# Performance work log

Measured on AMD Instinct MI355X. Metric: run time of the kernel, lower is better.

Reference implementation:

```python
import jax, jax.numpy as jnp
import numpy as np

B, T, E, H = 4, 1024, 1024, 16
D = E // H  # head_dim = 64


def setup_inputs() -> dict:
    key = jax.random.key(0)
    ks = jax.random.split(key, 6)
    s = 0.02  # realistic init scale for stable softmax
    return {
        "hidden_states": jax.random.normal(ks[0], (B, T, E), jnp.float32),
        "attention_mask": jnp.zeros((B, 1, T, T), jnp.float32),
        "Wq": jax.random.normal(ks[1], (E, E), jnp.float32) * s,
        "bq": jnp.zeros((E,), jnp.float32),
        "Wk": jax.random.normal(ks[2], (E, E), jnp.float32) * s,
        "bk": jnp.zeros((E,), jnp.float32),
        "Wv": jax.random.normal(ks[3], (E, E), jnp.float32) * s,
        "bv": jnp.zeros((E,), jnp.float32),
        "Wo": jax.random.normal(ks[4], (E, E), jnp.float32) * s,
        "bo": jnp.zeros((E,), jnp.float32),
    }


def reference(hidden_states, attention_mask, Wq, bq, Wk, bk, Wv, bv, Wo, bo):
    b, t, e = hidden_states.shape
    scaling = jnp.asarray(D, hidden_states.dtype) ** -0.5
    # q_proj weights/bias are pre-scaled in the module; equivalent to scaling q output
    q = (hidden_states @ Wq.T + bq) * scaling      # [B,T,E]
    k = hidden_states @ Wk.T + bk                   # self-attention path (no cache)
    v = hidden_states @ Wv.T + bv
    q = q.reshape(b, t, H, D)
    k = k.reshape(b, t, H, D)
    v = v.reshape(b, t, H, D)
    # bmm(q, k^T): [B,H,T,S] score matrix (materialized, as in the original)
    scores = jnp.einsum("bthd,bshd->bhts", q, k) + attention_mask
    probs = jax.nn.softmax(scores, axis=-1)
    ctx = jnp.einsum("bhts,bshd->bthd", probs, v).reshape(b, t, e)
    return ctx @ Wo.T + bo
```

## Files before the change

kernel.cpp:

```cpp
#include <hip/hip_runtime.h>
#include <math.h>

#define BB 4
#define TT 1024
#define EE 1024
#define HH 16
#define DD 64
#define KDIM 1024
#define N_HS (4096 * 1024)
#define N_W  (1024 * 1024)
#define NQKV (BB * HH * TT * DD)
#define LOG2E 1.44269504088896340736f

typedef _Float16 f16x8 __attribute__((ext_vector_type(8)));
typedef _Float16 f16x4 __attribute__((ext_vector_type(4)));
typedef _Float16 f16x2 __attribute__((ext_vector_type(2)));
typedef float    f32x4 __attribute__((ext_vector_type(4)));

__device__ __forceinline__ unsigned short f2h(float x) {
    _Float16 h = (_Float16)x;
    return __builtin_bit_cast(unsigned short, h);
}
__device__ __forceinline__ void split_h(float x, unsigned short& hi, unsigned short& lo) {
    _Float16 h = (_Float16)x;
    hi = __builtin_bit_cast(unsigned short, h);
    lo = f2h(x - (float)h);
}

__device__ __forceinline__ f16x2 cvt_pk(float a, float b) {
    return __builtin_bit_cast(f16x2, __builtin_amdgcn_cvt_pkrtz(a, b));
}

__device__ __forceinline__ void gload16(const void* g, void* l) {
    __builtin_amdgcn_global_load_lds(
        (const __attribute__((address_space(1))) void*)g,
        (__attribute__((address_space(3))) void*)l, 16, 0, 0);
}

__device__ __forceinline__ float mx3(float a, float b, float c) {
    return fmaxf(fmaxf(a, b), c);
}

__global__ __launch_bounds__(256)
void split_kernel(const float* __restrict__ hs,
                  const float* __restrict__ Wq, const float* __restrict__ Wk,
                  const float* __restrict__ Wv, const float* __restrict__ Wo,
                  const float* __restrict__ mask, int* __restrict__ mflag,
                  unsigned short* __restrict__ ws)
{
    const int u = blockIdx.x * 256 + threadIdx.x;
    if (u < (N_HS / 4) + N_W) {
        const float* src;
        unsigned short* dst;
        if (u < (N_HS / 4)) {
            src = hs + (size_t)u * 4;
            dst = ws + (size_t)u * 4;
        } else {
            int v = u - N_HS / 4;
            int wsel = v >> 18;
            int wo   = v & 0x3FFFF;
            const float* Wsrc = (wsel == 0) ? Wq : (wsel == 1) ? Wk : (wsel == 2) ? Wv : Wo;
            src = Wsrc + (size_t)wo * 4;
            dst = ws + (size_t)N_HS + (size_t)wsel * N_W + (size_t)wo * 4;
        }
        float4 x = *(const float4*)src;
        ushort4 h4;
        h4.x = f2h(x.x); h4.y = f2h(x.y); h4.z = f2h(x.z); h4.w = f2h(x.w);
        *(ushort4*)dst = h4;
    } else {
        int v = u - ((N_HS / 4) + N_W);
        float4 x = *(const float4*)(mask + (size_t)v * 4);
        bool nz = (x.x != 0.f) || (x.y != 0.f) || (x.z != 0.f) || (x.w != 0.f);
        if (__any(nz) && (threadIdx.x & 63) == 0)
            atomicOr(mflag, 1);
    }
}

__global__ __launch_bounds__(256)
void qkv_kernel(const unsigned short* __restrict__ hsp,
                const unsigned short* __restrict__ wqp,
                const float* __restrict__ bq, const float* __restrict__ bk,
                const float* __restrict__ bv,
                unsigned short* __restrict__ qkvb,
                unsigned short* __restrict__ vtp)
{
    __shared__ unsigned short Ah[128 * 32], Bh[128 * 32];
    __shared__ unsigned short Ts[128 * 128];

    const int widx  = blockIdx.x >> 3;
    const int nbase = (blockIdx.x & 7) * 128;
    const int mbase = blockIdx.y * 128;
    const unsigned short* Wp = wqp + (size_t)widx * N_W;
    const float* bias = (widx == 0) ? bq : (widx == 1) ? bk : bv;
    unsigned short* dst = qkvb + (size_t)widx * NQKV;
    const float scale = (widx == 0) ? 0.125f * LOG2E : 1.0f;

    const int tid  = threadIdx.x;
    const int w    = tid >> 6;
    const int lane = tid & 63;
    const int quad = lane >> 4;
    const int l16  = lane & 15;
    const int wm   = (w >> 1) * 64;
    const int wn   = (w & 1) * 64;

    f32x4 acc[4][4];
#pragma unroll
    for (int i = 0; i < 4; i++)
#pragma unroll
        for (int j = 0; j < 4; j++) acc[i][j] = (f32x4)0.f;

#pragma unroll 1
    for (int kt = 0; kt < KDIM; kt += 32) {
        __syncthreads();
#pragma unroll
        for (int i = 0; i < 2; i++) {
            int u = tid + i * 256;
            int r = u >> 2, c = u & 3;
            int q = c ^ ((r >> 1) & 3);
            gload16(hsp + (size_t)(mbase + r) * KDIM + kt + q * 8, &Ah[u * 8]);
            gload16(Wp  + (size_t)(nbase + r) * KDIM + kt + q * 8, &Bh[u * 8]);
        }
        __syncthreads();

        f16x8 af[4], bfr[4];
#pragma unroll
        for (int i = 0; i < 4; i++) {
            int r = wm + i * 16 + l16;
            af[i] = *(const f16x8*)&Ah[(r * 4 + (quad ^ ((r >> 1) & 3))) * 8];
        }
#pragma unroll
        for (int j = 0; j < 4; j++) {
            int r = wn + j * 16 + l16;
            bfr[j] = *(const f16x8*)&Bh[(r * 4 + (quad ^ ((r >> 1) & 3))) * 8];
        }
#pragma unroll
        for (int i = 0; i < 4; i++)
#pragma unroll
            for (int j = 0; j < 4; j++)
                acc[i][j] = __builtin_amdgcn_mfma_f32_16x16x32_f16(af[i], bfr[j], acc[i][j], 0, 0, 0);
    }

    if (widx == 2) {
#pragma unroll
        for (int j = 0; j < 4; j++) {
            int n = wn + j * 16 + l16;
            float bj = bias[nbase + n];
            int x = (n & 15) << 2;
#pragma unroll
            for (int i = 0; i < 4; i++) {
                int t4 = wm + i * 16 + quad * 4;
                ushort4 vw;
                vw.x = f2h(acc[i][j][0] + bj);
                vw.y = f2h(acc[i][j][1] + bj);
                vw.z = f2h(acc[i][j][2] + bj);
                vw.w = f2h(acc[i][j][3] + bj);
                *(ushort4*)&Ts[n * 128 + (t4 ^ x)] = vw;
            }
        }
        __syncthreads();
        const int b  = mbase >> 10;
        const int tb = mbase & 1023;
#pragma unroll
        for (int e = 0; e < 8; e++) {
            int c  = tid + e * 256;
            int n  = c >> 4, ch = c & 15;
            int x  = (n & 15) << 2;
            int s  = ch * 8;
            uint2 a0 = *(const uint2*)&Ts[n * 128 + (s ^ x)];
            uint2 a1 = *(const uint2*)&Ts[n * 128 + ((s + 4) ^ x)];
            int nn = nbase + n;
            int h = nn >> 6, d = nn & 63;
            uint4 o;
            o.x = a0.x; o.y = a0.y; o.z = a1.x; o.w = a1.y;
            *(uint4*)(vtp + (((size_t)(b * HH + h) * DD + d) * TT + tb + s)) = o;
        }
    } else {
#pragma unroll
        for (int j = 0; j < 4; j++) {
            int n = nbase + wn + j * 16 + l16;
            int h = n >> 6, d = n & 63;
            float bj = bias[n];
#pragma unroll
            for (int i = 0; i < 4; i++)
#pragma unroll
                for (int rr = 0; rr < 4; rr++) {
                    int m = mbase + wm + i * 16 + quad * 4 + rr;
                    int b = m >> 10, t = m & 1023;
                    dst[(((size_t)(b * HH + h) * TT + t) * DD + d)] =
                        f2h((acc[i][j][rr] + bj) * scale);
                }
        }
    }
}

__global__ __launch_bounds__(256)
void outproj_kernel(const unsigned short* __restrict__ ctxh,
                    const unsigned short* __restrict__ ctxl,
                    const unsigned short* __restrict__ wop,
                    const float* __restrict__ bo, float* __restrict__ out)
{
    __shared__ unsigned short Ach[64 * 32], Acl[64 * 32], Bh[128 * 32];

    const int nbase = blockIdx.x * 128;
    const int mbase = blockIdx.y * 64;

    const int tid  = threadIdx.x;
    const int w    = tid >> 6;
    const int lane = tid & 63;
    const int quad = lane >> 4;
    const int l16  = lane & 15;
    const int wm   = (w >> 1) * 32;
    const int wn   = (w & 1) * 64;

    f32x4 acc[2][4];
#pragma unroll
    for (int i = 0; i < 2; i++)
#pragma unroll
        for (int j = 0; j < 4; j++) acc[i][j] = (f32x4)0.f;

#pragma unroll 1
    for (int kt = 0; kt < KDIM; kt += 32) {
        __syncthreads();
        {
            int r = tid >> 2, c = tid & 3;
            int q = c ^ ((r >> 1) & 3);
            size_t ga = (size_t)(mbase + r) * KDIM + kt + q * 8;
            gload16(ctxh + ga, &Ach[tid * 8]);
            gload16(ctxl + ga, &Acl[tid * 8]);
        }
#pragma unroll
        for (int i = 0; i < 2; i++) {
            int u = tid + i * 256;
            int r = u >> 2, c = u & 3;
            int q = c ^ ((r >> 1) & 3);
            gload16(wop + (size_t)(nbase + r) * KDIM + kt + q * 8, &Bh[u * 8]);
        }
        __syncthreads();

        f16x8 ah[2], al[2], bfr[4];
#pragma unroll
        for (int i = 0; i < 2; i++) {
            int r = wm + i * 16 + l16;
            int slot = (r * 4 + (quad ^ ((r >> 1) & 3))) * 8;
            ah[i] = *(const f16x8*)&Ach[slot];
            al[i] = *(const f16x8*)&Acl[slot];
        }
#pragma unroll
        for (int j = 0; j < 4; j++) {
            int r = wn + j * 16 + l16;
            bfr[j] = *(const f16x8*)&Bh[(r * 4 + (quad ^ ((r >> 1) & 3))) * 8];
        }
#pragma unroll
        for (int i = 0; i < 2; i++)
#pragma unroll
            for (int j = 0; j < 4; j++) {
                acc[i][j] = __builtin_amdgcn_mfma_f32_16x16x32_f16(ah[i], bfr[j], acc[i][j], 0, 0, 0);
                acc[i][j] = __builtin_amdgcn_mfma_f32_16x16x32_f16(al[i], bfr[j], acc[i][j], 0, 0, 0);
            }
    }

#pragma unroll
    for (int j = 0; j < 4; j++) {
        int n = nbase + wn + j * 16 + l16;
        float bj = bo[n];
#pragma unroll
        for (int i = 0; i < 2; i++)
#pragma unroll
            for (int rr = 0; rr < 4; rr++) {
                int m = mbase + wm + i * 16 + quad * 4 + rr;
                out[(size_t)m * EE + n] = acc[i][j][rr] + bj;
            }
    }
}

__global__ __launch_bounds__(256)
void attn_kernel(const unsigned short* __restrict__ qp_, const unsigned short* __restrict__ kp_,
                 const unsigned short* __restrict__ vtp_,
                 const float* __restrict__ mask, const int* __restrict__ mflag,
                 unsigned short* __restrict__ ctxh, unsigned short* __restrict__ ctxl)
{
    __shared__ unsigned short Ks[2][64 * 64];
    __shared__ unsigned short Vt[2][64 * 64];

    const int bh = blockIdx.y;
    const int b  = bh >> 4;
    const int h  = bh & 15;
    const int m0 = blockIdx.x * 64;
    const size_t hoff = (size_t)bh * TT * DD;
    const unsigned short* qhp = qp_ + hoff;
    const unsigned short* khp = kp_ + hoff;
    const unsigned short* vtp = vtp_ + hoff;
    const float* mb = mask + (size_t)b * TT * TT;

    const int tid  = threadIdx.x;
    const int w    = tid >> 6;
    const int lane = tid & 63;
    const int quad = lane >> 4;
    const int l16  = lane & 15;
    const int m    = m0 + w * 16 + l16;

    const int usemask = mflag[0];

    const int lm7 = l16 & 7;
    const int x0  = l16 * 64 + ((quad)     ^ lm7) * 8;
    const int x1  = l16 * 64 + ((4 + quad) ^ lm7) * 8;
    const int qh  = quad >> 1, ql = quad & 1;
    int yy[4];
#pragma unroll
    for (int t = 0; t < 4; t++)
        yy[t] = l16 * 64 + ((2 * t + qh) ^ lm7) * 8 + ql * 4;
    const unsigned short* Ksf = &Ks[0][0];
    const unsigned short* Vtf = &Vt[0][0];

    f16x8 qf[2];
#pragma unroll
    for (int s = 0; s < 2; s++)
        qf[s] = *(const f16x8*)(qhp + (size_t)m * DD + s * 32 + quad * 8);

    f32x4 o2[4];
#pragma unroll
    for (int u = 0; u < 4; u++) o2[u] = (f32x4)0.f;
    f32x4 lv = (f32x4)0.f;
    const f32x4 zc = (f32x4)0.f;
    f16x4 onesv;
    onesv[0] = (_Float16)1.f; onesv[1] = (_Float16)1.f;
    onesv[2] = (_Float16)1.f; onesv[3] = (_Float16)1.f;
    float m_i = -INFINITY;

#pragma unroll
    for (int i = 0; i < 2; i++) {
        int u = tid + i * 256;
        int r = u >> 3, cp = u & 7;
        int c = cp ^ (r & 7);
        gload16(khp + (size_t)r * DD + c * 8, &Ks[0][u * 8]);
        gload16(vtp + (size_t)r * TT + c * 8, &Vt[0][u * 8]);
    }
    __syncthreads();

#pragma unroll 2
    for (int it = 0; it < 16; ++it) {
        const int n0  = it * 64;
        const int cur = it & 1;

        if (it < 15) {
#pragma unroll
            for (int i = 0; i < 2; i++) {
                int u = tid + i * 256;
                int r = u >> 3, cp = u & 7;
                int c = cp ^ (r & 7);
                gload16(khp + (size_t)(n0 + 64 + r) * DD + c * 8, &Ks[cur ^ 1][u * 8]);
                gload16(vtp + (size_t)r * TT + n0 + 64 + c * 8,   &Vt[cur ^ 1][u * 8]);
            }
        }

        f32x4 init[4];
        if (usemask) {
#pragma unroll
            for (int t = 0; t < 4; t++)
#pragma unroll
                for (int r = 0; r < 4; r++)
                    init[t][r] = mb[(size_t)m * TT + n0 + 16 * t + quad * 4 + r] * LOG2E;
        } else {
#pragma unroll
            for (int t = 0; t < 4; t++) init[t] = zc;
        }

        f32x4 st[4];
        __builtin_amdgcn_s_setprio(1);
#pragma unroll
        for (int t = 0; t < 4; t++) {
            const f16x8 kf = *(const f16x8*)(Ksf + cur * 4096 + x0 + t * 1024);
            st[t] = __builtin_amdgcn_mfma_f32_16x16x32_f16(kf, qf[0], init[t], 0, 0, 0);
        }
#pragma unroll
        for (int t = 0; t < 4; t++) {
            const f16x8 kf = *(const f16x8*)(Ksf + cur * 4096 + x1 + t * 1024);
            st[t] = __builtin_amdgcn_mfma_f32_16x16x32_f16(kf, qf[1], st[t], 0, 0, 0);
        }
        __builtin_amdgcn_s_setprio(0);

        float g0 = mx3(st[0][0], st[0][1], st[0][2]);
        float g1 = mx3(st[0][3], st[1][0], st[1][1]);
        float g2 = mx3(st[1][2], st[1][3], st[2][0]);
        float g3 = mx3(st[2][1], st[2][2], st[2][3]);
        float g4 = mx3(st[3][0], st[3][1], st[3][2]);
        float rm = fmaxf(mx3(g0, g1, g2), mx3(g3, g4, st[3][3]));
        rm = fmaxf(rm, __shfl_xor(rm, 16));
        rm = fmaxf(rm, __shfl_xor(rm, 32));

        if (__any(rm > m_i + 8.f)) {
            float mn    = fmaxf(m_i, rm);
            float alpha = exp2f(m_i - mn);
            m_i = mn;
#pragma unroll
            for (int rr = 0; rr < 4; rr++) lv[rr] *= alpha;
#pragma unroll
            for (int u = 0; u < 4; u++)
#pragma unroll
                for (int rr = 0; rr < 4; rr++) o2[u][rr] *= alpha;
        }

        f16x4 pb[4];
#pragma unroll
        for (int t = 0; t < 4; t++) {
            float p0 = exp2f(st[t][0] - m_i);
            float p1 = exp2f(st[t][1] - m_i);
            float p2 = exp2f(st[t][2] - m_i);
            float p3 = exp2f(st[t][3] - m_i);
            f16x2 plo = cvt_pk(p0, p1);
            f16x2 phi = cvt_pk(p2, p3);
            f16x4 pv;
            pv[0] = plo[0]; pv[1] = plo[1]; pv[2] = phi[0]; pv[3] = phi[1];
            pb[t] = pv;
        }

        __builtin_amdgcn_s_setprio(1);
#pragma unroll
        for (int t = 0; t < 4; t++)
            lv = __builtin_amdgcn_mfma_f32_16x16x16f16(onesv, pb[t], lv, 0, 0, 0);
#pragma unroll
        for (int u = 0; u < 4; u++) {
#pragma unroll
            for (int t = 0; t < 4; t++) {
                const f16x4 vv = *(const f16x4*)(Vtf + cur * 4096 + yy[t] + u * 1024);
                o2[u] = __builtin_amdgcn_mfma_f32_16x16x16f16(vv, pb[t], o2[u], 0, 0, 0);
            }
        }
        __builtin_amdgcn_s_setprio(0);

        __syncthreads();
    }

    float inv = 1.0f / lv[0];
#pragma unroll
    for (int u = 0; u < 4; u++)
#pragma unroll
        for (int rr = 0; rr < 4; rr++) {
            float val = o2[u][rr] * inv;
            unsigned short hi, lo;
            split_h(val, hi, lo);
            size_t off = ((size_t)(b * TT + m)) * EE + h * DD + u * 16 + quad * 4 + rr;
            ctxh[off] = hi;
            ctxl[off] = lo;
        }
}

extern "C" void kernel_launch(void* const* d_in, const int* in_sizes, int n_in,
                              void* d_out, int out_size, void* d_ws, size_t ws_size,
                              hipStream_t stream)
{
    const float* hs   = (const float*)d_in[0];
    const float* mask = (const float*)d_in[1];
    const float* Wq   = (const float*)d_in[2];
    const float* bq   = (const float*)d_in[3];
    const float* Wk   = (const float*)d_in[4];
    const float* bk   = (const float*)d_in[5];
    const float* Wv   = (const float*)d_in[6];
    const float* bv   = (const float*)d_in[7];
    const float* Wo   = (const float*)d_in[8];
    const float* bo   = (const float*)d_in[9];
    float* out = (float*)d_out;

    unsigned short* ws   = (unsigned short*)d_ws;
    unsigned short* hsp  = ws;
    unsigned short* wqp  = ws + (size_t)N_HS;
    unsigned short* wop  = wqp + 3 * (size_t)N_W;
    unsigned short* qkvb = wqp + 4 * (size_t)N_W;
    unsigned short* qp   = qkvb;
    unsigned short* kp   = qp + (size_t)NQKV;
    unsigned short* ctxh = ws;
    unsigned short* ctxl = qkvb + 3 * (size_t)NQKV;
    unsigned short* vtp  = ctxl + (size_t)N_HS;
    int*            mflag = (int*)(vtp + (size_t)NQKV);

    (void)hipMemsetAsync(mflag, 0, sizeof(int), stream);
    split_kernel<<<12288, 256, 0, stream>>>(hs, Wq, Wk, Wv, Wo, mask, mflag, ws);
    qkv_kernel<<<dim3(24, 32), 256, 0, stream>>>(hsp, wqp, bq, bk, bv, qkvb, vtp);
    attn_kernel<<<dim3(TT / 64, BB * HH), 256, 0, stream>>>(qp, kp, vtp, mask, mflag, ctxh, ctxl);
    outproj_kernel<<<dim3(8, 64), 256, 0, stream>>>(ctxh, ctxl, wop, bo, out);
}
```

Baseline: 229.7 us.

## Process two query row-groups per wave in attention and alias qkv shared buffers

Each attention wave now handles 32 query rows (two 16-row groups) instead of 16, so a block covers 128 queries and every K/V tile loaded into shared memory is reused across twice as many rows, with half as many blocks launched. The qkv kernel folds its A/B staging buffers and transpose buffer into one aliased shared array, adding a barrier before the transpose writes, to cut LDS use. The trade-off is more registers per wave in attention and fewer blocks, which may lower occupancy and latency hiding.

```diff
diff --git a/kernel.cpp b/kernel.cpp
--- a/kernel.cpp
+++ b/kernel.cpp
@@ -84,8 +84,10 @@
                 unsigned short* __restrict__ qkvb,
                 unsigned short* __restrict__ vtp)
 {
-    __shared__ unsigned short Ah[128 * 32], Bh[128 * 32];
-    __shared__ unsigned short Ts[128 * 128];
+    __shared__ unsigned short qbuf[128 * 128];
+    unsigned short* Ah = qbuf;
+    unsigned short* Bh = qbuf + 4096;
+    unsigned short* Ts = qbuf;
 
     const int widx  = blockIdx.x >> 3;
     const int nbase = (blockIdx.x & 7) * 128;
@@ -141,6 +143,7 @@
     }
 
     if (widx == 2) {
+        __syncthreads();
 #pragma unroll
         for (int j = 0; j < 4; j++) {
             int n = wn + j * 16 + l16;
@@ -285,7 +288,7 @@
     const int bh = blockIdx.y;
     const int b  = bh >> 4;
     const int h  = bh & 15;
-    const int m0 = blockIdx.x * 64;
+    const int m0 = blockIdx.x * 128;
     const size_t hoff = (size_t)bh * TT * DD;
     const unsigned short* qhp = qp_ + hoff;
     const unsigned short* khp = kp_ + hoff;
@@ -297,7 +300,7 @@
     const int lane = tid & 63;
     const int quad = lane >> 4;
     const int l16  = lane & 15;
-    const int m    = m0 + w * 16 + l16;
+    const int mw   = m0 + w * 32;
 
     const int usemask = mflag[0];
 
@@ -312,20 +315,25 @@
     const unsigned short* Ksf = &Ks[0][0];
     const unsigned short* Vtf = &Vt[0][0];
 
-    f16x8 qf[2];
-#pragma unroll
-    for (int s = 0; s < 2; s++)
-        qf[s] = *(const f16x8*)(qhp + (size_t)m * DD + s * 32 + quad * 8);
-
-    f32x4 o2[4];
-#pragma unroll
-    for (int u = 0; u < 4; u++) o2[u] = (f32x4)0.f;
-    f32x4 lv = (f32x4)0.f;
+    f16x8 qf[2][2];
+#pragma unroll
+    for (int g = 0; g < 2; g++)
+#pragma unroll
+        for (int s = 0; s < 2; s++)
+            qf[g][s] = *(const f16x8*)(qhp + (size_t)(mw + g * 16 + l16) * DD + s * 32 + quad * 8);
+
+    f32x4 o2[2][4];
+#pragma unroll
+    for (int g = 0; g < 2; g++)
+#pragma unroll
+        for (int u = 0; u < 4; u++) o2[g][u] = (f32x4)0.f;
+    f32x4 lv[2];
+    lv[0] = (f32x4)0.f; lv[1] = (f32x4)0.f;
     const f32x4 zc = (f32x4)0.f;
     f16x4 onesv;
     onesv[0] = (_Float16)1.f; onesv[1] = (_Float16)1.f;
     onesv[2] = (_Float16)1.f; onesv[3] = (_Float16)1.f;
-    float m_i = -INFINITY;
+    float m_i[2] = { -INFINITY, -INFINITY };
 
 #pragma unroll
     for (int i = 0; i < 2; i++) {
@@ -353,77 +361,88 @@
             }
         }
 
-        f32x4 init[4];
+        f32x4 st[2][4];
         if (usemask) {
 #pragma unroll
-            for (int t = 0; t < 4; t++)
-#pragma unroll
-                for (int r = 0; r < 4; r++)
-                    init[t][r] = mb[(size_t)m * TT + n0 + 16 * t + quad * 4 + r] * LOG2E;
+            for (int g = 0; g < 2; g++)
+#pragma unroll
+                for (int t = 0; t < 4; t++)
+#pragma unroll
+                    for (int r = 0; r < 4; r++)
+                        st[g][t][r] = mb[(size_t)(mw + g * 16 + l16) * TT + n0 + 16 * t + quad * 4 + r] * LOG2E;
         } else {
 #pragma unroll
-            for (int t = 0; t < 4; t++) init[t] = zc;
-        }
-
-        f32x4 st[4];
+            for (int g = 0; g < 2; g++)
+#pragma unroll
+                for (int t = 0; t < 4; t++) st[g][t] = zc;
+        }
+
         __builtin_amdgcn_s_setprio(1);
 #pragma unroll
         for (int t = 0; t < 4; t++) {
             const f16x8 kf = *(const f16x8*)(Ksf + cur * 4096 + x0 + t * 1024);
-            st[t] = __builtin_amdgcn_mfma_f32_16x16x32_f16(kf, qf[0], init[t], 0, 0, 0);
+            st[0][t] = __builtin_amdgcn_mfma_f32_16x16x32_f16(kf, qf[0][0], st[0][t], 0, 0, 0);
+            st[1][t] = __builtin_amdgcn_mfma_f32_16x16x32_f16(kf, qf[1][0], st[1][t], 0, 0, 0);
         }
 #pragma unroll
         for (int t = 0; t < 4; t++) {
             const f16x8 kf = *(const f16x8*)(Ksf + cur * 4096 + x1 + t * 1024);
-            st[t] = __builtin_amdgcn_mfma_f32_16x16x32_f16(kf, qf[1], st[t], 0, 0, 0);
+            st[0][t] = __builtin_amdgcn_mfma_f32_16x16x32_f16(kf, qf[0][1], st[0][t], 0, 0, 0);
+            st[1][t] = __builtin_amdgcn_mfma_f32_16x16x32_f16(kf, qf[1][1], st[1][t], 0, 0, 0);
         }
         __builtin_amdgcn_s_setprio(0);
 
-        float g0 = mx3(st[0][0], st[0][1], st[0][2]);
-        float g1 = mx3(st[0][3], st[1][0], st[1][1]);
-        float g2 = mx3(st[1][2], st[1][3], st[2][0]);
-        float g3 = mx3(st[2][1], st[2][2], st[2][3]);
-        float g4 = mx3(st[3][0], st[3][1], st[3][2]);
-        float rm = fmaxf(mx3(g0, g1, g2), mx3(g3, g4, st[3][3]));
-        rm = fmaxf(rm, __shfl_xor(rm, 16));
-        rm = fmaxf(rm, __shfl_xor(rm, 32));
-
-        if (__any(rm > m_i + 8.f)) {
-            float mn    = fmaxf(m_i, rm);
-            float alpha = exp2f(m_i - mn);
-            m_i = mn;
-#pragma unroll
-            for (int rr = 0; rr < 4; rr++) lv[rr] *= alpha;
-#pragma unroll
-            for (int u = 0; u < 4; u++)
-#pragma unroll
-                for (int rr = 0; rr < 4; rr++) o2[u][rr] *= alpha;
-        }
-
-        f16x4 pb[4];
+        f16x4 pb[2][4];
+#pragma unroll
+        for (int g = 0; g < 2; g++) {
+            float g0 = mx3(st[g][0][0], st[g][0][1], st[g][0][2]);
+            float g1 = mx3(st[g][0][3], st[g][1][0], st[g][1][1]);
+            float g2 = mx3(st[g][1][2], st[g][1][3], st[g][2][0]);
+            float g3 = mx3(st[g][2][1], st[g][2][2], st[g][2][3]);
+            float g4 = mx3(st[g][3][0], st[g][3][1], st[g][3][2]);
+            float rm = fmaxf(mx3(g0, g1, g2), mx3(g3, g4, st[g][3][3]));
+            rm = fmaxf(rm, __shfl_xor(rm, 16));
+            rm = fmaxf(rm, __shfl_xor(rm, 32));
+
+            if (__any(rm > m_i[g] + 8.f)) {
+                float mn    = fmaxf(m_i[g], rm);
+                float alpha = exp2f(m_i[g] - mn);
+                m_i[g] = mn;
+#pragma unroll
+                for (int rr = 0; rr < 4; rr++) lv[g][rr] *= alpha;
+#pragma unroll
+                for (int u = 0; u < 4; u++)
+#pragma unroll
+                    for (int rr = 0; rr < 4; rr++) o2[g][u][rr] *= alpha;
+            }
+
+#pragma unroll
+            for (int t = 0; t < 4; t++) {
+                float p0 = exp2f(st[g][t][0] - m_i[g]);
+                float p1 = exp2f(st[g][t][1] - m_i[g]);
+                float p2 = exp2f(st[g][t][2] - m_i[g]);
+                float p3 = exp2f(st[g][t][3] - m_i[g]);
+                f16x2 plo = cvt_pk(p0, p1);
+                f16x2 phi = cvt_pk(p2, p3);
+                f16x4 pv;
+                pv[0] = plo[0]; pv[1] = plo[1]; pv[2] = phi[0]; pv[3] = phi[1];
+                pb[g][t] = pv;
+            }
+        }
+
+        __builtin_amdgcn_s_setprio(1);
 #pragma unroll
         for (int t = 0; t < 4; t++) {
-            float p0 = exp2f(st[t][0] - m_i);
-            float p1 = exp2f(st[t][1] - m_i);
-            float p2 = exp2f(st[t][2] - m_i);
-            float p3 = exp2f(st[t][3] - m_i);
-            f16x2 plo = cvt_pk(p0, p1);
-            f16x2 phi = cvt_pk(p2, p3);
-            f16x4 pv;
-            pv[0] = plo[0]; pv[1] = plo[1]; pv[2] = phi[0]; pv[3] = phi[1];
-            pb[t] = pv;
-        }
-
-        __builtin_amdgcn_s_setprio(1);
-#pragma unroll
-        for (int t = 0; t < 4; t++)
-            lv = __builtin_amdgcn_mfma_f32_16x16x16f16(onesv, pb[t], lv, 0, 0, 0);
+            lv[0] = __builtin_amdgcn_mfma_f32_16x16x16f16(onesv, pb[0][t], lv[0], 0, 0, 0);
+            lv[1] = __builtin_amdgcn_mfma_f32_16x16x16f16(onesv, pb[1][t], lv[1], 0, 0, 0);
+        }
 #pragma unroll
         for (int u = 0; u < 4; u++) {
 #pragma unroll
             for (int t = 0; t < 4; t++) {
                 const f16x4 vv = *(const f16x4*)(Vtf + cur * 4096 + yy[t] + u * 1024);
-                o2[u] = __builtin_amdgcn_mfma_f32_16x16x16f16(vv, pb[t], o2[u], 0, 0, 0);
+                o2[0][u] = __builtin_amdgcn_mfma_f32_16x16x16f16(vv, pb[0][t], o2[0][u], 0, 0, 0);
+                o2[1][u] = __builtin_amdgcn_mfma_f32_16x16x16f16(vv, pb[1][t], o2[1][u], 0, 0, 0);
             }
         }
         __builtin_amdgcn_s_setprio(0);
@@ -431,18 +450,22 @@
         __syncthreads();
     }
 
-    float inv = 1.0f / lv[0];
-#pragma unroll
-    for (int u = 0; u < 4; u++)
-#pragma unroll
-        for (int rr = 0; rr < 4; rr++) {
-            float val = o2[u][rr] * inv;
-            unsigned short hi, lo;
-            split_h(val, hi, lo);
-            size_t off = ((size_t)(b * TT + m)) * EE + h * DD + u * 16 + quad * 4 + rr;
-            ctxh[off] = hi;
-            ctxl[off] = lo;
-        }
+#pragma unroll
+    for (int g = 0; g < 2; g++) {
+        float inv = 1.0f / lv[g][0];
+        int m = mw + g * 16 + l16;
+#pragma unroll
+        for (int u = 0; u < 4; u++)
+#pragma unroll
+            for (int rr = 0; rr < 4; rr++) {
+                float val = o2[g][u][rr] * inv;
+                unsigned short hi, lo;
+                split_h(val, hi, lo);
+                size_t off = ((size_t)(b * TT + m)) * EE + h * DD + u * 16 + quad * 4 + rr;
+                ctxh[off] = hi;
+                ctxl[off] = lo;
+            }
+    }
 }
 
 extern "C" void kernel_launch(void* const* d_in, const int* in_sizes, int n_in,
@@ -476,6 +499,6 @@
     (void)hipMemsetAsync(mflag, 0, sizeof(int), stream);
     split_kernel<<<12288, 256, 0, stream>>>(hs, Wq, Wk, Wv, Wo, mask, mflag, ws);
     qkv_kernel<<<dim3(24, 32), 256, 0, stream>>>(hsp, wqp, bq, bk, bv, qkvb, vtp);
-    attn_kernel<<<dim3(TT / 64, BB * HH), 256, 0, stream>>>(qp, kp, vtp, mask, mflag, ctxh, ctxl);
+    attn_kernel<<<dim3(TT / 128, BB * HH), 256, 0, stream>>>(qp, kp, vtp, mask, mflag, ctxh, ctxl);
     outproj_kernel<<<dim3(8, 64), 256, 0, stream>>>(ctxh, ctxl, wop, bo, out);
 }
```

Result: no change. 233.3 us (+1.5%).
